# Kernel optimization log

Hardware: AMD Instinct MI355X
Metric: run time of the kernel (lower is better)

The kernel has to match this reference:

```python
import jax, jax.numpy as jnp
import numpy as np

B, S, H2, TOPIC = 32, 1024, 1024, 256  # hidden_dim*2 = 1024


def setup_inputs() -> dict:
    key = jax.random.key(0)
    ks = jax.random.split(key, 9)
    sc = 1.0 / np.sqrt(H2)
    return {
        "encoder_features": jax.random.normal(ks[0], (B, S, H2), jnp.float32),
        "mask": jnp.ones((B, S), jnp.int32),
        "s": jax.random.normal(ks[1], (B, H2), jnp.float32),
        "coverage": jax.random.uniform(ks[2], (B, S), jnp.float32),
        "hidden_z": jax.random.normal(ks[3], (B, TOPIC), jnp.float32),
        # learned params (torch Linear stores weight as [out, in]; we use [in, out])
        "W_s": jax.random.normal(ks[4], (H2, H2), jnp.float32) * sc,
        "W_c": jax.random.normal(ks[5], (1, H2), jnp.float32) * sc,
        "b_c": jax.random.normal(ks[6], (H2,), jnp.float32) * sc,
        "W_z": jax.random.normal(ks[7], (TOPIC, H2), jnp.float32) * sc,
        "v": jax.random.normal(ks[8], (H2,), jnp.float32) * sc,
    }


def reference(encoder_features, mask, s, coverage, hidden_z, W_s, W_c, b_c, W_z, v):
    # decoder feature: [B, 1, 2H]
    dec = (s @ W_s)[:, None, :]
    # coverage feature: [B, S, 2H] (w_c has bias)
    cov = coverage[:, :, None] * W_c[0] + b_c
    # topic feature: [B, 1, 2H]
    top = (hidden_z @ W_z)[:, None, :]
    feat = encoder_features + dec + cov + top          # [B, S, 2H]
    e_t = jnp.einsum('bsh,h->bs', jnp.tanh(feat), v)    # [B, S]
    e_t = jnp.where(mask == 0, -jnp.inf, e_t)
    a_t = jax.nn.softmax(e_t, axis=-1)                  # [B, S]
    next_coverage = coverage + a_t
    return (a_t, next_coverage)
```

## Files before the change

### kernel.cpp

```cpp
#include <hip/hip_runtime.h>
#include <math.h>

#define B_     32
#define S_     1024
#define H2_    1024
#define TOPIC_ 256

__device__ __forceinline__ float fast_tanh(float x) {
    float e = __expf(2.0f * x);
    return 1.0f - 2.0f / (e + 1.0f);
}

__global__ __launch_bounds__(256) void combined_kernel(
    const float* __restrict__ s,
    const float* __restrict__ hz,
    const float* __restrict__ W_s,
    const float* __restrict__ W_z,
    const float* __restrict__ b_c,
    float* __restrict__ combined)
{
    const int b  = blockIdx.y;
    const int hl = threadIdx.x & 31;
    const int h  = blockIdx.x * 32 + hl;
    const int kc = threadIdx.x >> 5;

    __shared__ float sx[H2_];
    __shared__ float zx[TOPIC_];
    for (int i = threadIdx.x; i < H2_; i += 256)    sx[i] = s[b * H2_ + i];
    for (int i = threadIdx.x; i < TOPIC_; i += 256) zx[i] = hz[b * TOPIC_ + i];
    __syncthreads();

    float a0 = 0.f, a1 = 0.f, a2 = 0.f, a3 = 0.f;
    {
        const int k0 = kc * 128;
        const float* Wp = W_s + (size_t)k0 * H2_ + h;
        #pragma unroll 4
        for (int i = 0; i < 128; i += 4) {
            a0 = fmaf(sx[k0 + i    ], Wp[(size_t)(i    ) * H2_], a0);
            a1 = fmaf(sx[k0 + i + 1], Wp[(size_t)(i + 1) * H2_], a1);
            a2 = fmaf(sx[k0 + i + 2], Wp[(size_t)(i + 2) * H2_], a2);
            a3 = fmaf(sx[k0 + i + 3], Wp[(size_t)(i + 3) * H2_], a3);
        }
    }
    {
        const int j0 = kc * 32;
        const float* Wp = W_z + (size_t)j0 * H2_ + h;
        #pragma unroll 4
        for (int i = 0; i < 32; i += 4) {
            a0 = fmaf(zx[j0 + i    ], Wp[(size_t)(i    ) * H2_], a0);
            a1 = fmaf(zx[j0 + i + 1], Wp[(size_t)(i + 1) * H2_], a1);
            a2 = fmaf(zx[j0 + i + 2], Wp[(size_t)(i + 2) * H2_], a2);
            a3 = fmaf(zx[j0 + i + 3], Wp[(size_t)(i + 3) * H2_], a3);
        }
    }
    const float acc = (a0 + a1) + (a2 + a3);

    __shared__ float part[8][32];
    part[kc][hl] = acc;
    __syncthreads();
    if (kc == 0) {
        float r = b_c[h];
        #pragma unroll
        for (int c = 0; c < 8; ++c) r += part[c][hl];
        combined[b * H2_ + h] = r;
    }
}

__global__ __launch_bounds__(256, 4) void et_kernel(
    const float* __restrict__ enc,
    const float* __restrict__ coverage,
    const float* __restrict__ W_c,
    const float* __restrict__ v,
    const float* __restrict__ combined,
    float* __restrict__ e_out)
{
    const int tid  = threadIdx.x;
    const int row  = blockIdx.x * 4 + (tid >> 6);
    const int b    = row >> 10;
    const int lane = tid & 63;

    const float4* e4   = (const float4*)enc + (size_t)row * (H2_ / 4);
    const float4* com4 = (const float4*)(combined + (size_t)b * H2_);
    const float4* wc4  = (const float4*)W_c;
    const float4* v4   = (const float4*)v;

    const float cov = coverage[row];

    float acc = 0.0f;
    #pragma unroll
    for (int i = 0; i < 4; ++i) {
        const int idx = lane + i * 64;
        const float4 e  = e4[idx];
        const float4 w  = wc4[idx];
        const float4 vv = v4[idx];
        const float4 cb = com4[idx];
        acc = fmaf(fast_tanh(fmaf(cov, w.x, e.x) + cb.x), vv.x, acc);
        acc = fmaf(fast_tanh(fmaf(cov, w.y, e.y) + cb.y), vv.y, acc);
        acc = fmaf(fast_tanh(fmaf(cov, w.z, e.z) + cb.z), vv.z, acc);
        acc = fmaf(fast_tanh(fmaf(cov, w.w, e.w) + cb.w), vv.w, acc);
    }

    #pragma unroll
    for (int off = 32; off > 0; off >>= 1)
        acc += __shfl_xor(acc, off, 64);

    if (lane == 0)
        e_out[row] = acc;
}

__global__ __launch_bounds__(256) void softmax_kernel(
    const float* __restrict__ e_in,
    const int*   __restrict__ mask,
    const float* __restrict__ coverage,
    float* __restrict__ a_out,
    float* __restrict__ cov_out)
{
    const int b   = blockIdx.x;
    const int tid = threadIdx.x;

    float ev[4];
    #pragma unroll
    for (int i = 0; i < 4; ++i) {
        const int idx = b * S_ + tid * 4 + i;
        float e = e_in[idx];
        if (mask[idx] == 0) e = -INFINITY;
        ev[i] = e;
    }

    float m = fmaxf(fmaxf(ev[0], ev[1]), fmaxf(ev[2], ev[3]));
    #pragma unroll
    for (int off = 1; off < 64; off <<= 1)
        m = fmaxf(m, __shfl_xor(m, off, 64));

    __shared__ float red[4];
    if ((tid & 63) == 0) red[tid >> 6] = m;
    __syncthreads();
    m = fmaxf(fmaxf(red[0], red[1]), fmaxf(red[2], red[3]));

    float p[4];
    float lsum = 0.0f;
    #pragma unroll
    for (int i = 0; i < 4; ++i) {
        p[i] = __expf(ev[i] - m);
        lsum += p[i];
    }
    #pragma unroll
    for (int off = 1; off < 64; off <<= 1)
        lsum += __shfl_xor(lsum, off, 64);

    __syncthreads();
    if ((tid & 63) == 0) red[tid >> 6] = lsum;
    __syncthreads();
    const float tot = red[0] + red[1] + red[2] + red[3];
    const float inv = 1.0f / tot;

    #pragma unroll
    for (int i = 0; i < 4; ++i) {
        const int idx = b * S_ + tid * 4 + i;
        const float a = p[i] * inv;
        a_out[idx]   = a;
        cov_out[idx] = coverage[idx] + a;
    }
}

extern "C" void kernel_launch(void* const* d_in, const int* in_sizes, int n_in,
                              void* d_out, int out_size, void* d_ws, size_t ws_size,
                              hipStream_t stream) {
    const float* enc      = (const float*)d_in[0];
    const int*   mask     = (const int*)  d_in[1];
    const float* s        = (const float*)d_in[2];
    const float* coverage = (const float*)d_in[3];
    const float* hz       = (const float*)d_in[4];
    const float* W_s      = (const float*)d_in[5];
    const float* W_c      = (const float*)d_in[6];
    const float* b_c      = (const float*)d_in[7];
    const float* W_z      = (const float*)d_in[8];
    const float* v        = (const float*)d_in[9];

    float* out_a   = (float*)d_out;
    float* out_cov = out_a + B_ * S_;

    float* combined = (float*)d_ws;
    float* e_ws     = combined + B_ * H2_;

    combined_kernel<<<dim3(H2_ / 32, B_), 256, 0, stream>>>(s, hz, W_s, W_z, b_c, combined);
    et_kernel<<<(B_ * S_) / 4, 256, 0, stream>>>(enc, coverage, W_c, v, combined, e_ws);
    softmax_kernel<<<B_, 256, 0, stream>>>(e_ws, mask, coverage, out_a, out_cov);
}
```

Baseline: 38.51 us.

## Process eight rows per wave in et_kernel, reusing per-column weights in registers

Each wave now handles eight encoder rows, two at a time, instead of one. The W_c, v and combined vectors are loaded into registers once and reused across those rows, and the grid is reduced eightfold. This removes redundant weight and combined loads and puts two independent row loads in flight per iteration. In exchange there are fewer blocks to hide memory latency, the row loop is serialized with unroll 1, and register pressure rises.

```diff
diff --git a/kernel.cpp b/kernel.cpp
--- a/kernel.cpp
+++ b/kernel.cpp
@@ -75,37 +75,63 @@
     float* __restrict__ e_out)
 {
     const int tid  = threadIdx.x;
-    const int row  = blockIdx.x * 4 + (tid >> 6);
-    const int b    = row >> 10;
+    const int wv   = tid >> 6;
     const int lane = tid & 63;
-
-    const float4* e4   = (const float4*)enc + (size_t)row * (H2_ / 4);
+    const int row0 = blockIdx.x * 32 + wv * 8;
+    const int b    = row0 >> 10;
+
     const float4* com4 = (const float4*)(combined + (size_t)b * H2_);
     const float4* wc4  = (const float4*)W_c;
     const float4* v4   = (const float4*)v;
 
-    const float cov = coverage[row];
-
-    float acc = 0.0f;
+    float4 wc[4], vv[4], cb[4];
     #pragma unroll
     for (int i = 0; i < 4; ++i) {
         const int idx = lane + i * 64;
-        const float4 e  = e4[idx];
-        const float4 w  = wc4[idx];
-        const float4 vv = v4[idx];
-        const float4 cb = com4[idx];
-        acc = fmaf(fast_tanh(fmaf(cov, w.x, e.x) + cb.x), vv.x, acc);
-        acc = fmaf(fast_tanh(fmaf(cov, w.y, e.y) + cb.y), vv.y, acc);
-        acc = fmaf(fast_tanh(fmaf(cov, w.z, e.z) + cb.z), vv.z, acc);
-        acc = fmaf(fast_tanh(fmaf(cov, w.w, e.w) + cb.w), vv.w, acc);
-    }
-
-    #pragma unroll
-    for (int off = 32; off > 0; off >>= 1)
-        acc += __shfl_xor(acc, off, 64);
-
-    if (lane == 0)
-        e_out[row] = acc;
+        wc[i] = wc4[idx];
+        vv[i] = v4[idx];
+        cb[i] = com4[idx];
+    }
+
+    #pragma unroll 1
+    for (int rp = 0; rp < 8; rp += 2) {
+        const int ra = row0 + rp;
+        const int rb = ra + 1;
+        const float4* ea = (const float4*)enc + (size_t)ra * (H2_ / 4);
+        const float4* eb = (const float4*)enc + (size_t)rb * (H2_ / 4);
+        const float cva = coverage[ra];
+        const float cvb = coverage[rb];
+
+        float4 La[4], Lb[4];
+        #pragma unroll
+        for (int i = 0; i < 4; ++i) {
+            La[i] = ea[lane + i * 64];
+            Lb[i] = eb[lane + i * 64];
+        }
+
+        float aca = 0.0f, acb = 0.0f;
+        #pragma unroll
+        for (int i = 0; i < 4; ++i) {
+            aca = fmaf(fast_tanh(fmaf(cva, wc[i].x, La[i].x + cb[i].x)), vv[i].x, aca);
+            aca = fmaf(fast_tanh(fmaf(cva, wc[i].y, La[i].y + cb[i].y)), vv[i].y, aca);
+            aca = fmaf(fast_tanh(fmaf(cva, wc[i].z, La[i].z + cb[i].z)), vv[i].z, aca);
+            aca = fmaf(fast_tanh(fmaf(cva, wc[i].w, La[i].w + cb[i].w)), vv[i].w, aca);
+            acb = fmaf(fast_tanh(fmaf(cvb, wc[i].x, Lb[i].x + cb[i].x)), vv[i].x, acb);
+            acb = fmaf(fast_tanh(fmaf(cvb, wc[i].y, Lb[i].y + cb[i].y)), vv[i].y, acb);
+            acb = fmaf(fast_tanh(fmaf(cvb, wc[i].z, Lb[i].z + cb[i].z)), vv[i].z, acb);
+            acb = fmaf(fast_tanh(fmaf(cvb, wc[i].w, Lb[i].w + cb[i].w)), vv[i].w, acb);
+        }
+
+        #pragma unroll
+        for (int off = 32; off > 0; off >>= 1) {
+            aca += __shfl_xor(aca, off, 64);
+            acb += __shfl_xor(acb, off, 64);
+        }
+        if (lane == 0) {
+            e_out[ra] = aca;
+            e_out[rb] = acb;
+        }
+    }
 }
 
 __global__ __launch_bounds__(256) void softmax_kernel(
@@ -184,6 +210,6 @@
     float* e_ws     = combined + B_ * H2_;
 
     combined_kernel<<<dim3(H2_ / 32, B_), 256, 0, stream>>>(s, hz, W_s, W_z, b_c, combined);
-    et_kernel<<<(B_ * S_) / 4, 256, 0, stream>>>(enc, coverage, W_c, v, combined, e_ws);
+    et_kernel<<<(B_ * S_) / 32, 256, 0, stream>>>(enc, coverage, W_c, v, combined, e_ws);
     softmax_kernel<<<B_, 256, 0, stream>>>(e_ws, mask, coverage, out_a, out_cov);
 }
```

Result: slower. 42.05 us (+9.2%).
